# Performance work log

Hardware: AMD Instinct MI355X
Metric: run time of the kernel (lower is better)

Reference implementation:

```python
import jax, jax.numpy as jnp
import numpy as np

B, T, V, E, H, L = 64, 512, 100, 100, 256, 8


def _lstm_layer(xs, w_ih, w_hh, b_ih, b_hh):
    # xs: [B, T, I]; PyTorch gate order: i, f, g, o
    gx = jnp.einsum('bti,gi->btg', xs, w_ih) + b_ih  # [B, T, 4H]
    gx = jnp.swapaxes(gx, 0, 1)                      # [T, B, 4H]
    w_hh_t = w_hh.T                                  # [H, 4H]
    h0 = jnp.zeros((xs.shape[0], w_hh.shape[1]), xs.dtype)

    def step(carry, g):
        h, c = carry
        g = g + h @ w_hh_t + b_hh
        i, f, gg, o = jnp.split(g, 4, axis=-1)
        c = jax.nn.sigmoid(f) * c + jax.nn.sigmoid(i) * jnp.tanh(gg)
        h = jax.nn.sigmoid(o) * jnp.tanh(c)
        return (h, c), h

    (hT, cT), ys = jax.lax.scan(step, (h0, h0), gx)
    return jnp.swapaxes(ys, 0, 1), hT, cT


def setup_inputs() -> dict:
    key = jax.random.key(0)
    ks = jax.random.split(key, 9)
    s = 0.05  # roughly PyTorch's 1/sqrt(H) uniform scale
    return {
        'x': jax.random.randint(ks[0], (B, T), 0, V),
        'embed': jax.random.normal(ks[1], (V, E), jnp.float32) * s,
        'w_ih0': jax.random.normal(ks[2], (4 * H, E), jnp.float32) * s,
        'w_ih': jax.random.normal(ks[3], (L - 1, 4 * H, H), jnp.float32) * s,
        'w_hh': jax.random.normal(ks[4], (L, 4 * H, H), jnp.float32) * s,
        'b_ih': jax.random.normal(ks[5], (L, 4 * H), jnp.float32) * s,
        'b_hh': jax.random.normal(ks[6], (L, 4 * H), jnp.float32) * s,
        'fc_w': jax.random.normal(ks[7], (V, H), jnp.float32) * s,
        'fc_b': jax.random.normal(ks[8], (V,), jnp.float32) * s,
    }


def reference(x, embed, w_ih0, w_ih, w_hh, b_ih, b_hh, fc_w, fc_b):
    h = embed[x]  # [B, T, E]
    h_fin, c_fin = [], []
    for l in range(L):
        wih = w_ih0 if l == 0 else w_ih[l - 1]
        h, hT, cT = _lstm_layer(h, wih, w_hh[l], b_ih[l], b_hh[l])
        h_fin.append(hT)
        c_fin.append(cT)
    logits = jnp.einsum('bth,vh->btv', h, fc_w) + fc_b  # [B, T, V]
    return logits, jnp.stack(h_fin), jnp.stack(c_fin)
```

## Files before the change

kernel.cpp:

```cpp
#include <hip/hip_runtime.h>


typedef _Float16 f16;
typedef f16  f16x8 __attribute__((ext_vector_type(8)));
typedef f16  f16x4 __attribute__((ext_vector_type(4)));
typedef float f32x4 __attribute__((ext_vector_type(4)));
typedef int   i32x4 __attribute__((ext_vector_type(4)));

#define DEV __device__ __forceinline__

constexpr int TT = 512, BB = 64, VV = 100, HH = 256, LL = 8;
constexpr int RING_D = 32;
constexpr int POISON = 0x7C007C00;
constexpr int MAXRETRY = 4096;

constexpr size_t XE_OFF = 0;
constexpr size_t XE_SZ  = (size_t)TT*BB*256*2;
constexpr size_t WP_OFF = XE_OFF + XE_SZ;
constexpr size_t WP_SZ  = (size_t)LL*16*64*512*2;
constexpr size_t BI_OFF = WP_OFF + WP_SZ;
constexpr size_t BI_SZ  = (size_t)LL*16*64*4;
constexpr size_t FW_OFF = BI_OFF + BI_SZ;
constexpr size_t FW_SZ  = (size_t)112*256*2;
constexpr size_t H7_OFF = FW_OFF + FW_SZ;
constexpr size_t H7_SZ  = (size_t)TT*BB*256*2;
constexpr size_t RG_OFF = H7_OFF + H7_SZ;
constexpr size_t RG_SZ  = (size_t)LL*RING_D*BB*256*2;
constexpr size_t FCF_OFF = RG_OFF + RG_SZ;
constexpr size_t FCF_SZ  = (size_t)7*TT*16;

DEV void ld16_pl (i32x4& d, const void* p){ asm volatile("global_load_dwordx4 %0, %1, off"     : "=v"(d) : "v"(p)); }
DEV void ld16_sc1(i32x4& d, const void* p){ asm volatile("global_load_dwordx4 %0, %1, off sc1" : "=v"(d) : "v"(p)); }
DEV void st16_sc1(void* p, i32x4 d){ asm volatile("global_store_dwordx4 %0, %1, off sc1" :: "v"(p), "v"(d) : "memory"); }
DEV void stb_sc1(void* p){ unsigned o = 1; asm volatile("global_store_byte %0, %1, off sc1" :: "v"(p), "v"(o) : "memory"); }
DEV void wait_vm0(){ asm volatile("s_waitcnt vmcnt(0)" ::: "memory"); __builtin_amdgcn_sched_barrier(0); }
DEV void wait_vm8(){ asm volatile("s_waitcnt vmcnt(8)" ::: "memory"); __builtin_amdgcn_sched_barrier(0); }

DEV bool chk8(const i32x4* f) {
  int bad = 0;
  #pragma unroll
  for (int i = 0; i < 8; ++i) {
    bad |= (f[i][0] == POISON);
    bad |= (f[i][1] == POISON);
    bad |= (f[i][2] == POISON);
    bad |= (f[i][3] == POISON);
  }
  return __all(bad == 0);
}

DEV bool poll16(const unsigned char* p) {
  for (int it = 0; it < (1 << 16); ++it) {
    i32x4 f;
    asm volatile("global_load_dwordx4 %0, %1, off sc1\n\ts_waitcnt vmcnt(0)"
                 : "=v"(f) : "v"(p) : "memory");
    if ((f[0] & f[1] & f[2] & f[3]) == 0x01010101) return true;
    if (it > 2) __builtin_amdgcn_s_sleep(1);
  }
  return false;
}

DEV float sig2(float y)  { return __builtin_amdgcn_rcpf(1.f + __builtin_amdgcn_exp2f(-y)); }
DEV float tanhp(float y) { return 1.f - 2.f * __builtin_amdgcn_rcpf(1.f + __builtin_amdgcn_exp2f(y)); }
constexpr float LOG2E = 1.4426950408889634f;
constexpr float C2LE  = 2.8853900817779268f;
DEV unsigned f16bits(float v) { f16 h = (f16)v; return (unsigned)__builtin_bit_cast(unsigned short, h); }

__global__ void prep_zero(unsigned int* p) {
  p[blockIdx.x * 256 + threadIdx.x] = 0;
}
__global__ void prep_poison(unsigned int* p) {
  size_t i = ((size_t)blockIdx.x * 256 + threadIdx.x) * 4;
  i32x4 P = {POISON, POISON, POISON, POISON};
  *(i32x4*)(p + i) = P;
}

__global__ void prep_embed(const int* __restrict__ x, const float* __restrict__ em,
                           f16* __restrict__ xe) {
  int g = blockIdx.x * 256 + threadIdx.x;
  int chunk = g & 7, pair = g >> 3;
  int b = pair & 63, t = pair >> 6;
  int idx = x[b * 512 + t];
  const float* er = em + (size_t)idx * 100;
  f16* o = xe + (size_t)pair * 256 + chunk * 32;
  #pragma unroll
  for (int c4 = 0; c4 < 32; c4 += 4) {
    f16x4 v;
    #pragma unroll
    for (int q = 0; q < 4; ++q) {
      int c = chunk * 32 + c4 + q;
      v[q] = (c < 100) ? (f16)er[c] : (f16)0.f;
    }
    *(f16x4*)(o + c4) = v;
  }
}

__global__ void prep_w(const float* __restrict__ w_ih0, const float* __restrict__ w_ih,
                       const float* __restrict__ w_hh, f16* __restrict__ wpo) {
  int g = blockIdx.x * 256 + threadIdx.x;
  int k4 = (g & 127) * 4;
  int n  = (g >> 7) & 63;
  int ls = g >> 13;
  int l = ls >> 4, s = ls & 15;
  int gate = n & 3;
  int u = s * 16 + ((n >> 4) << 2) + ((n >> 2) & 3);
  int r = 256 * gate + u;
  float scale = (gate == 2) ? C2LE : LOG2E;
  f16x4 v;
  #pragma unroll
  for (int q = 0; q < 4; ++q) {
    int k = k4 + q;
    float f;
    if (k < 256) {
      if (l == 0) f = (k < 100) ? w_ih0[(size_t)r * 100 + k] : 0.f;
      else        f = w_ih[((size_t)(l - 1) * 1024 + r) * 256 + k];
    } else        f = w_hh[((size_t)l * 1024 + r) * 256 + (k - 256)];
    v[q] = (f16)(f * scale);
  }
  *(f16x4*)(wpo + (size_t)g * 4) = v;
}

__global__ void prep_bias(const float* __restrict__ b_ih, const float* __restrict__ b_hh,
                          float* __restrict__ bo) {
  int g = blockIdx.x * 256 + threadIdx.x;
  int n = g & 63, s = (g >> 6) & 15, l = g >> 10;
  int gate = n & 3;
  int u = s * 16 + ((n >> 4) << 2) + ((n >> 2) & 3);
  int r = 256 * gate + u;
  float scale = (gate == 2) ? C2LE : LOG2E;
  bo[g] = (b_ih[l * 1024 + r] + b_hh[l * 1024 + r]) * scale;
}

__global__ void prep_fcw(const float* __restrict__ fc_w, f16* __restrict__ fo) {
  int g = blockIdx.x * 256 + threadIdx.x;
  int n = g >> 6, k4 = (g & 63) * 4;
  f16x4 v;
  #pragma unroll
  for (int q = 0; q < 4; ++q)
    v[q] = (n < 100) ? (f16)fc_w[(size_t)n * 256 + k4 + q] : (f16)0.f;
  *(f16x4*)(fo + (size_t)g * 4) = v;
}

__global__ void __launch_bounds__(512, 1) lstm_pipe(
    const f16* __restrict__ xe, const f16* __restrict__ wp, const float* __restrict__ biasp,
    f16* h7, f16* rings, unsigned char* fcf, float* out)
{
  __shared__ char pad_lds[40960];
  __shared__ unsigned short pub[2][64][24];
  (void)((volatile char*)pad_lds)[threadIdx.x];

  const int bx  = blockIdx.x;
  const int lyr = bx & 7;
  const int sl  = bx >> 3;
  const int tid = threadIdx.x;
  const int wv  = tid >> 6;
  const int ln  = tid & 63;
  const int mA  = wv >> 2;
  const int nB  = wv & 3;

  f16x8 wfa[2][16];
  {
    const f16* wb = wp + (size_t)(lyr * 16 + sl) * 64 * 512;
    #pragma unroll
    for (int tt = 0; tt < 2; ++tt)
      #pragma unroll
      for (int kt = 0; kt < 16; ++kt) {
        wfa[tt][kt] = *(const f16x8*)(wb + (size_t)((2 * mA + tt) * 16 + (ln & 15)) * 512
                                      + kt * 32 + (ln >> 4) * 8);
        i32x4 pin = __builtin_bit_cast(i32x4, wfa[tt][kt]);
        asm volatile("" : "+v"(pin));
        wfa[tt][kt] = __builtin_bit_cast(f16x8, pin);
      }
  }
  f32x4 bias_v[2];
  #pragma unroll
  for (int tt = 0; tt < 2; ++tt) {
    bias_v[tt] = *(const f32x4*)(biasp + (size_t)(lyr * 16 + sl) * 64
                                 + (2 * mA + tt) * 16 + (ln >> 4) * 4);
    asm volatile("" : "+v"(bias_v[tt]));
  }

  float cst0 = 0.f, cst1 = 0.f;
  const int q    = ln >> 4;
  const int bcol = nB * 16 + (ln & 15);
  const int kof  = q * 8;
  const f16* xring = rings + (size_t)(lyr - 1) * RING_D * 16384;
  f16*       hring = rings + (size_t)lyr * RING_D * 16384;
  bool dead = false;

  for (int t = 0; t < TT; ++t) {
    if (wv == 0 && t + 1 < TT) {
      if (lyr < 7 && t + 1 >= RING_D && !dead)
        dead = !poll16(fcf + (size_t)(lyr * TT + (t + 1 - RING_D)) * 16);
      f16* pz = hring + (size_t)((t + 1) & (RING_D - 1)) * 16384
              + (size_t)ln * 256 + sl * 16;
      i32x4 P = {POISON, POISON, POISON, POISON};
      st16_sc1(pz, P);
      st16_sc1(pz + 8, P);
    }

    const bool hasH = (t > 0);
    i32x4 bfx[8], bfh[8];
    {
      const f16* xb = ((lyr == 0) ? xe + (size_t)t * 16384
                                  : xring + (size_t)(t & (RING_D - 1)) * 16384)
                      + (size_t)bcol * 256 + kof;
      if (lyr == 0) {
        #pragma unroll
        for (int kt = 0; kt < 8; ++kt) ld16_pl(bfx[kt], xb + kt * 32);
      } else {
        #pragma unroll
        for (int kt = 0; kt < 8; ++kt) ld16_sc1(bfx[kt], xb + kt * 32);
      }
      if (hasH) {
        const f16* hb = hring + (size_t)((t - 1) & (RING_D - 1)) * 16384
                      + (size_t)bcol * 256 + kof;
        #pragma unroll
        for (int kt = 0; kt < 8; ++kt) ld16_sc1(bfh[kt], hb + kt * 32);
      }
    }
    if (hasH) wait_vm8(); else wait_vm0();

    if (lyr > 0 && !dead) {
      int it = 0;
      while (!chk8(bfx)) {
        if (++it > MAXRETRY) { dead = true; break; }
        wait_vm0();
        const f16* xb = xring + (size_t)(t & (RING_D - 1)) * 16384
                      + (size_t)bcol * 256 + kof;
        #pragma unroll
        for (int kt = 0; kt < 8; ++kt) ld16_sc1(bfx[kt], xb + kt * 32);
        wait_vm0();
      }
    }

    f32x4 acc0 = {0,0,0,0}, acc1 = {0,0,0,0};
    #pragma unroll
    for (int kt = 0; kt < 8; ++kt) {
      f16x8 av = __builtin_bit_cast(f16x8, bfx[kt]);
      acc0 = __builtin_amdgcn_mfma_f32_16x16x32_f16(wfa[0][kt], av, acc0, 0, 0, 0);
      acc1 = __builtin_amdgcn_mfma_f32_16x16x32_f16(wfa[1][kt], av, acc1, 0, 0, 0);
    }

    if (hasH) {
      wait_vm0();
      if (!dead) {
        int it = 0;
        while (!chk8(bfh)) {
          if (++it > MAXRETRY) { dead = true; break; }
          const f16* hb = hring + (size_t)((t - 1) & (RING_D - 1)) * 16384
                        + (size_t)bcol * 256 + kof;
          #pragma unroll
          for (int kt = 0; kt < 8; ++kt) ld16_sc1(bfh[kt], hb + kt * 32);
          wait_vm0();
        }
      }
      #pragma unroll
      for (int kt = 0; kt < 8; ++kt) {
        f16x8 av = __builtin_bit_cast(f16x8, bfh[kt]);
        acc0 = __builtin_amdgcn_mfma_f32_16x16x32_f16(wfa[0][8 + kt], av, acc0, 0, 0, 0);
        acc1 = __builtin_amdgcn_mfma_f32_16x16x32_f16(wfa[1][8 + kt], av, acc1, 0, 0, 0);
      }
    }

    const int par = t & 1;
    #pragma unroll
    for (int tt = 0; tt < 2; ++tt) {
      f32x4 g4 = (tt == 0 ? acc0 : acc1);
      g4 += bias_v[tt];
      float i_ = sig2(g4[0]), f_ = sig2(g4[1]), z_ = tanhp(g4[2]), o_ = sig2(g4[3]);
      float& c_ = (tt == 0 ? cst0 : cst1);
      c_ = f_ * c_ + i_ * z_;
      float h_ = o_ * tanhp(c_ * C2LE);
      pub[par][bcol][(2 * mA + tt) * 4 + q] = (unsigned short)f16bits(h_);
      if (t == TT - 1) {
        const int u = sl * 16 + (2 * mA + tt) * 4 + q;
        size_t ob = 3276800 + (size_t)lyr * 16384 + (size_t)bcol * 256 + u;
        out[ob] = h_;  out[ob + 131072] = c_;
      }
    }
    __syncthreads();

    if (wv == 0) {
      i32x4 d0 = *(const i32x4*)&pub[par][ln][0];
      i32x4 d1 = *(const i32x4*)&pub[par][ln][8];
      f16* dst = hring + (size_t)(t & (RING_D - 1)) * 16384 + (size_t)ln * 256 + sl * 16;
      st16_sc1(dst, d0);
      st16_sc1(dst + 8, d1);
      if (lyr == 7) {
        f16* hd = h7 + (size_t)t * 16384 + (size_t)ln * 256 + sl * 16;
        *(i32x4*)hd = d0;
        *(i32x4*)(hd + 8) = d1;
      }
      if (ln == 1 && lyr > 0)
        stb_sc1(fcf + (size_t)((lyr - 1) * TT + t) * 16 + sl);
    }
  }
}

__global__ void __launch_bounds__(256, 1) fc_kernel(
    const f16* __restrict__ h7, const f16* __restrict__ fcw,
    const float* __restrict__ fcb, float* __restrict__ out)
{
  const int t  = blockIdx.x;
  const int wv = threadIdx.x >> 6;
  const int ln = threadIdx.x & 63;
  const f16* ab = h7 + (size_t)t * 16384 + (size_t)(wv * 16 + (ln & 15)) * 256 + (ln >> 4) * 8;
  f16x8 af[8];
  #pragma unroll
  for (int kt = 0; kt < 8; ++kt) af[kt] = *(const f16x8*)(ab + kt * 32);
  const int obrow = wv * 16 + (ln >> 4) * 4;
  #pragma unroll
  for (int nt = 0; nt < 7; ++nt) {
    const f16* bb = fcw + (size_t)(nt * 16 + (ln & 15)) * 256 + (ln >> 4) * 8;
    f32x4 acc = {0, 0, 0, 0};
    #pragma unroll
    for (int kt = 0; kt < 8; ++kt) {
      f16x8 bv = *(const f16x8*)(bb + kt * 32);
      acc = __builtin_amdgcn_mfma_f32_16x16x32_f16(af[kt], bv, acc, 0, 0, 0);
    }
    int vg = nt * 16 + (ln & 15);
    if (vg < VV) {
      float bias = fcb[vg];
      #pragma unroll
      for (int j = 0; j < 4; ++j)
        out[(size_t)(obrow + j) * 51200 + (size_t)t * 100 + vg] = acc[j] + bias;
    }
  }
}

extern "C" void kernel_launch(void* const* d_in, const int* in_sizes, int n_in,
                              void* d_out, int out_size, void* d_ws, size_t ws_size,
                              hipStream_t stream) {
  (void)in_sizes; (void)n_in; (void)out_size; (void)ws_size;
  const int*   x     = (const int*)d_in[0];
  const float* embed = (const float*)d_in[1];
  const float* w_ih0 = (const float*)d_in[2];
  const float* w_ih  = (const float*)d_in[3];
  const float* w_hh  = (const float*)d_in[4];
  const float* b_ih  = (const float*)d_in[5];
  const float* b_hh  = (const float*)d_in[6];
  const float* fc_w  = (const float*)d_in[7];
  const float* fc_b  = (const float*)d_in[8];
  char* ws = (char*)d_ws;
  float* out = (float*)d_out;

  prep_zero<<<56, 256, 0, stream>>>((unsigned int*)(ws + FCF_OFF));
  prep_poison<<<2048, 256, 0, stream>>>((unsigned int*)(ws + RG_OFF));
  prep_embed<<<1024, 256, 0, stream>>>(x, embed, (f16*)(ws + XE_OFF));
  prep_w<<<4096, 256, 0, stream>>>(w_ih0, w_ih, w_hh, (f16*)(ws + WP_OFF));
  prep_bias<<<32, 256, 0, stream>>>(b_ih, b_hh, (float*)(ws + BI_OFF));
  prep_fcw<<<28, 256, 0, stream>>>(fc_w, (f16*)(ws + FW_OFF));

  lstm_pipe<<<128, 512, 35072, stream>>>(
      (const f16*)(ws + XE_OFF), (const f16*)(ws + WP_OFF), (const float*)(ws + BI_OFF),
      (f16*)(ws + H7_OFF), (f16*)(ws + RG_OFF),
      (unsigned char*)(ws + FCF_OFF), out);

  fc_kernel<<<512, 256, 0, stream>>>((const f16*)(ws + H7_OFF), (const f16*)(ws + FW_OFF),
                                     fc_b, out);
}
```

Measured before the change: 3.117 ms.

## Split hidden-state ring per layer and use XCD-local cache scope when colocated

Each layer's 16 workgroups read the XCC_ID hardware register and run a handshake to check whether they all landed on the same XCD. If they did, the recurrent h ring is stored and loaded with sc0 (workgroup/L2-local scope) instead of sc1 (system-coherent). A separate x-ring is kept with sc1 for handoff to the next layer, which may sit on another XCD. This is meant to cut the latency of the serial per-timestep recurrence, at the cost of duplicate stores each step and reliance on the hardware's placement of workgroups.

```diff
diff --git a/kernel.cpp b/kernel.cpp
--- a/kernel.cpp
+++ b/kernel.cpp
@@ -24,15 +24,24 @@
 constexpr size_t FW_SZ  = (size_t)112*256*2;
 constexpr size_t H7_OFF = FW_OFF + FW_SZ;
 constexpr size_t H7_SZ  = (size_t)TT*BB*256*2;
-constexpr size_t RG_OFF = H7_OFF + H7_SZ;
-constexpr size_t RG_SZ  = (size_t)LL*RING_D*BB*256*2;
-constexpr size_t FCF_OFF = RG_OFF + RG_SZ;
+constexpr size_t HR_OFF = H7_OFF + H7_SZ;
+constexpr size_t HR_SZ  = (size_t)LL*RING_D*BB*256*2;
+constexpr size_t XR_OFF = HR_OFF + HR_SZ;
+constexpr size_t XR_SZ  = (size_t)7*RING_D*BB*256*2;
+constexpr size_t FCF_OFF = XR_OFF + XR_SZ;
 constexpr size_t FCF_SZ  = (size_t)7*TT*16;
+constexpr size_t XC_OFF  = FCF_OFF + FCF_SZ;
+constexpr size_t XC_SZ   = 128;
+constexpr int ZERO_DW = (int)((FCF_SZ + XC_SZ) / 4);
+constexpr int POIS_TH = (int)((HR_SZ + XR_SZ) / 16);
 
 DEV void ld16_pl (i32x4& d, const void* p){ asm volatile("global_load_dwordx4 %0, %1, off"     : "=v"(d) : "v"(p)); }
+DEV void ld16_sc0(i32x4& d, const void* p){ asm volatile("global_load_dwordx4 %0, %1, off sc0" : "=v"(d) : "v"(p)); }
 DEV void ld16_sc1(i32x4& d, const void* p){ asm volatile("global_load_dwordx4 %0, %1, off sc1" : "=v"(d) : "v"(p)); }
+DEV void st16_sc0(void* p, i32x4 d){ asm volatile("global_store_dwordx4 %0, %1, off sc0" :: "v"(p), "v"(d) : "memory"); }
 DEV void st16_sc1(void* p, i32x4 d){ asm volatile("global_store_dwordx4 %0, %1, off sc1" :: "v"(p), "v"(d) : "memory"); }
 DEV void stb_sc1(void* p){ unsigned o = 1; asm volatile("global_store_byte %0, %1, off sc1" :: "v"(p), "v"(o) : "memory"); }
+DEV void stb_val_sc1(void* p, unsigned v){ asm volatile("global_store_byte %0, %1, off sc1" :: "v"(p), "v"(v) : "memory"); }
 DEV void wait_vm0(){ asm volatile("s_waitcnt vmcnt(0)" ::: "memory"); __builtin_amdgcn_sched_barrier(0); }
 DEV void wait_vm8(){ asm volatile("s_waitcnt vmcnt(8)" ::: "memory"); __builtin_amdgcn_sched_barrier(0); }
 
@@ -59,14 +68,30 @@
   return false;
 }
 
+DEV bool hs_poll(const unsigned char* p) {
+  for (int it = 0; it < (1 << 20); ++it) {
+    i32x4 f;
+    asm volatile("global_load_dwordx4 %0, %1, off sc1\n\ts_waitcnt vmcnt(0)"
+                 : "=v"(f) : "v"(p) : "memory");
+    int a = f[0] & f[1] & f[2] & f[3];
+    if ((a & 0x10101010) == 0x10101010) {
+      int e = (f[0] & 0xFF) * 0x01010101;
+      return f[0] == e && f[1] == e && f[2] == e && f[3] == e;
+    }
+    __builtin_amdgcn_s_sleep(1);
+  }
+  return false;
+}
+
 DEV float sig2(float y)  { return __builtin_amdgcn_rcpf(1.f + __builtin_amdgcn_exp2f(-y)); }
 DEV float tanhp(float y) { return 1.f - 2.f * __builtin_amdgcn_rcpf(1.f + __builtin_amdgcn_exp2f(y)); }
 constexpr float LOG2E = 1.4426950408889634f;
 constexpr float C2LE  = 2.8853900817779268f;
 DEV unsigned f16bits(float v) { f16 h = (f16)v; return (unsigned)__builtin_bit_cast(unsigned short, h); }
 
-__global__ void prep_zero(unsigned int* p) {
-  p[blockIdx.x * 256 + threadIdx.x] = 0;
+__global__ void prep_zero(unsigned int* p, int n) {
+  int i = blockIdx.x * 256 + threadIdx.x;
+  if (i < n) p[i] = 0;
 }
 __global__ void prep_poison(unsigned int* p) {
   size_t i = ((size_t)blockIdx.x * 256 + threadIdx.x) * 4;
@@ -142,7 +167,7 @@
 
 __global__ void __launch_bounds__(512, 1) lstm_pipe(
     const f16* __restrict__ xe, const f16* __restrict__ wp, const float* __restrict__ biasp,
-    f16* h7, f16* rings, unsigned char* fcf, float* out)
+    f16* h7, f16* hrg, f16* xrg, unsigned char* fcf, unsigned char* xc, float* out)
 {
   __shared__ char pad_lds[40960];
   __shared__ unsigned short pub[2][64][24];
@@ -179,23 +204,36 @@
     asm volatile("" : "+v"(bias_v[tt]));
   }
 
+  unsigned xcc = 0;
+  asm volatile("s_getreg_b32 %0, hwreg(20, 0, 32)" : "=s"(xcc));
+  unsigned char* xcg = xc + lyr * 16;
+  if (tid == 0) stb_val_sc1(xcg + sl, 0x10 | (xcc & 15));
+  const bool fast = hs_poll(xcg);
+
   float cst0 = 0.f, cst1 = 0.f;
   const int q    = ln >> 4;
   const int bcol = nB * 16 + (ln & 15);
   const int kof  = q * 8;
-  const f16* xring = rings + (size_t)(lyr - 1) * RING_D * 16384;
-  f16*       hring = rings + (size_t)lyr * RING_D * 16384;
+  const f16* xring = xrg + (size_t)(lyr - 1) * RING_D * 16384;
+  f16*       xdst  = xrg + (size_t)lyr * RING_D * 16384;
+  f16*       hring = hrg + (size_t)lyr * RING_D * 16384;
   bool dead = false;
 
   for (int t = 0; t < TT; ++t) {
     if (wv == 0 && t + 1 < TT) {
       if (lyr < 7 && t + 1 >= RING_D && !dead)
         dead = !poll16(fcf + (size_t)(lyr * TT + (t + 1 - RING_D)) * 16);
+      i32x4 P = {POISON, POISON, POISON, POISON};
       f16* pz = hring + (size_t)((t + 1) & (RING_D - 1)) * 16384
               + (size_t)ln * 256 + sl * 16;
-      i32x4 P = {POISON, POISON, POISON, POISON};
-      st16_sc1(pz, P);
-      st16_sc1(pz + 8, P);
+      if (fast) { st16_sc0(pz, P); st16_sc0(pz + 8, P); }
+      else      { st16_sc1(pz, P); st16_sc1(pz + 8, P); }
+      if (lyr < 7) {
+        f16* px = xdst + (size_t)((t + 1) & (RING_D - 1)) * 16384
+                + (size_t)ln * 256 + sl * 16;
+        st16_sc1(px, P);
+        st16_sc1(px + 8, P);
+      }
     }
 
     const bool hasH = (t > 0);
@@ -214,8 +252,13 @@
       if (hasH) {
         const f16* hb = hring + (size_t)((t - 1) & (RING_D - 1)) * 16384
                       + (size_t)bcol * 256 + kof;
-        #pragma unroll
-        for (int kt = 0; kt < 8; ++kt) ld16_sc1(bfh[kt], hb + kt * 32);
+        if (fast) {
+          #pragma unroll
+          for (int kt = 0; kt < 8; ++kt) ld16_sc0(bfh[kt], hb + kt * 32);
+        } else {
+          #pragma unroll
+          for (int kt = 0; kt < 8; ++kt) ld16_sc1(bfh[kt], hb + kt * 32);
+        }
       }
     }
     if (hasH) wait_vm8(); else wait_vm0();
@@ -249,8 +292,13 @@
           if (++it > MAXRETRY) { dead = true; break; }
           const f16* hb = hring + (size_t)((t - 1) & (RING_D - 1)) * 16384
                         + (size_t)bcol * 256 + kof;
-          #pragma unroll
-          for (int kt = 0; kt < 8; ++kt) ld16_sc1(bfh[kt], hb + kt * 32);
+          if (fast) {
+            #pragma unroll
+            for (int kt = 0; kt < 8; ++kt) ld16_sc0(bfh[kt], hb + kt * 32);
+          } else {
+            #pragma unroll
+            for (int kt = 0; kt < 8; ++kt) ld16_sc1(bfh[kt], hb + kt * 32);
+          }
           wait_vm0();
         }
       }
@@ -283,13 +331,17 @@
     if (wv == 0) {
       i32x4 d0 = *(const i32x4*)&pub[par][ln][0];
       i32x4 d1 = *(const i32x4*)&pub[par][ln][8];
-      f16* dst = hring + (size_t)(t & (RING_D - 1)) * 16384 + (size_t)ln * 256 + sl * 16;
-      st16_sc1(dst, d0);
-      st16_sc1(dst + 8, d1);
-      if (lyr == 7) {
-        f16* hd = h7 + (size_t)t * 16384 + (size_t)ln * 256 + sl * 16;
-        *(i32x4*)hd = d0;
-        *(i32x4*)(hd + 8) = d1;
+      f16* hd = hring + (size_t)(t & (RING_D - 1)) * 16384 + (size_t)ln * 256 + sl * 16;
+      if (fast) { st16_sc0(hd, d0); st16_sc0(hd + 8, d1); }
+      else      { st16_sc1(hd, d0); st16_sc1(hd + 8, d1); }
+      if (lyr < 7) {
+        f16* xd = xdst + (size_t)(t & (RING_D - 1)) * 16384 + (size_t)ln * 256 + sl * 16;
+        st16_sc1(xd, d0);
+        st16_sc1(xd + 8, d1);
+      } else {
+        f16* h7d = h7 + (size_t)t * 16384 + (size_t)ln * 256 + sl * 16;
+        *(i32x4*)h7d = d0;
+        *(i32x4*)(h7d + 8) = d1;
       }
       if (ln == 1 && lyr > 0)
         stb_sc1(fcf + (size_t)((lyr - 1) * TT + t) * 16 + sl);
@@ -344,8 +396,8 @@
   char* ws = (char*)d_ws;
   float* out = (float*)d_out;
 
-  prep_zero<<<56, 256, 0, stream>>>((unsigned int*)(ws + FCF_OFF));
-  prep_poison<<<2048, 256, 0, stream>>>((unsigned int*)(ws + RG_OFF));
+  prep_zero<<<57, 256, 0, stream>>>((unsigned int*)(ws + FCF_OFF), ZERO_DW);
+  prep_poison<<<POIS_TH / 256, 256, 0, stream>>>((unsigned int*)(ws + HR_OFF));
   prep_embed<<<1024, 256, 0, stream>>>(x, embed, (f16*)(ws + XE_OFF));
   prep_w<<<4096, 256, 0, stream>>>(w_ih0, w_ih, w_hh, (f16*)(ws + WP_OFF));
   prep_bias<<<32, 256, 0, stream>>>(b_ih, b_hh, (float*)(ws + BI_OFF));
@@ -353,8 +405,8 @@
 
   lstm_pipe<<<128, 512, 35072, stream>>>(
       (const f16*)(ws + XE_OFF), (const f16*)(ws + WP_OFF), (const float*)(ws + BI_OFF),
-      (f16*)(ws + H7_OFF), (f16*)(ws + RG_OFF),
-      (unsigned char*)(ws + FCF_OFF), out);
+      (f16*)(ws + H7_OFF), (f16*)(ws + HR_OFF), (f16*)(ws + XR_OFF),
+      (unsigned char*)(ws + FCF_OFF), (unsigned char*)(ws + XC_OFF), out);
 
   fc_kernel<<<512, 256, 0, stream>>>((const f16*)(ws + H7_OFF), (const f16*)(ws + FW_OFF),
                                      fc_b, out);
```

Result: slower. 3.215 ms (+3.2%).
